# Kernel optimization log

Measured on AMD Instinct MI355X. Metric: run time of the kernel, lower is better.

The kernel has to match this reference:

```python
import jax, jax.numpy as jnp
import numpy as np

N_HEADS = 16
HEAD_DIM = 64
ROPE_BASE = 10000.0


def _rope_cos_sin(T, d, dtype):
    # GPT-NeoX style: inv_freq over even indices, cos/sin duplicated to full head_dim
    inv_freq = 1.0 / (ROPE_BASE ** (jnp.arange(0, d, 2, dtype=jnp.float32) / d))
    freqs = jnp.arange(T, dtype=jnp.float32)[:, None] * inv_freq[None, :]  # [T, d/2]
    emb = jnp.concatenate([freqs, freqs], axis=-1)  # [T, d]
    return jnp.cos(emb).astype(dtype), jnp.sin(emb).astype(dtype)


def _rotate_half(x):
    x1, x2 = jnp.split(x, 2, axis=-1)
    return jnp.concatenate([-x2, x1], axis=-1)


def setup_inputs() -> dict:
    key = jax.random.key(0)
    k1, k2, k3 = jax.random.split(key, 3)
    B, T, C = 2, 2048, 1024
    x = jax.random.normal(k1, (B, T, C), dtype=jnp.float32)
    Wqkv = jax.random.normal(k2, (C, 3 * C), dtype=jnp.float32) * (1.0 / np.sqrt(C))
    Wout = jax.random.normal(k3, (C, C), dtype=jnp.float32) * (1.0 / np.sqrt(C))
    return {"x": x, "Wqkv": Wqkv, "Wout": Wout}


def reference(x, Wqkv, Wout):
    B, T, C = x.shape
    H, D = N_HEADS, HEAD_DIM
    qkv = (x @ Wqkv).reshape(B, T, 3, H, D)
    q, k, v = qkv[:, :, 0], qkv[:, :, 1], qkv[:, :, 2]  # [B,T,H,D]
    q = q.transpose(0, 2, 1, 3)  # [B,H,T,D]
    k = k.transpose(0, 2, 1, 3)
    v = v.transpose(0, 2, 1, 3)
    cos, sin = _rope_cos_sin(T, D, x.dtype)  # [T,D]
    cos = cos[None, None]
    sin = sin[None, None]
    q = q * cos + _rotate_half(q) * sin
    k = k * cos + _rotate_half(k) * sin
    scale = 1.0 / np.sqrt(D)
    scores = jnp.einsum("bhqd,bhkd->bhqk", q, k) * scale  # [B,H,T,T]
    causal = jnp.tril(jnp.ones((T, T), dtype=bool))
    scores = jnp.where(causal[None, None], scores, jnp.finfo(scores.dtype).min)
    attn = jax.nn.softmax(scores, axis=-1)
    out = jnp.einsum("bhqk,bhkd->bhqd", attn, v)  # [B,H,T,D]
    out = out.transpose(0, 2, 1, 3).reshape(B, T, C)
    return out @ Wout
```

## Files before the change

kernel.cpp:

```cpp
#include <hip/hip_runtime.h>


#define B_  2
#define T_  2048
#define C_  1024
#define H_  16
#define D_  64
#define N3_ 3072

typedef unsigned short ushortx8 __attribute__((ext_vector_type(8)));
typedef unsigned short ushortx4 __attribute__((ext_vector_type(4)));
typedef short bf16x8 __attribute__((ext_vector_type(8)));
typedef float f32x4 __attribute__((ext_vector_type(4)));
typedef float f32x16 __attribute__((ext_vector_type(16)));
typedef unsigned int uintx2 __attribute__((ext_vector_type(2)));

__device__ __forceinline__ unsigned short f2bf(float f) {
  union { float f; unsigned u; } v; v.f = f;
  unsigned r = v.u + 0x7FFFu + ((v.u >> 16) & 1u);
  return (unsigned short)(r >> 16);
}
__device__ __forceinline__ float bf2f(unsigned short h) {
  union { unsigned u; float f; } v; v.u = ((unsigned)h) << 16;
  return v.f;
}
__device__ __forceinline__ unsigned cvtpk_bf16(float lo, float hi) {
  unsigned r; asm("v_cvt_pk_bf16_f32 %0, %1, %2" : "=v"(r) : "v"(lo), "v"(hi));
  return r;
}
__device__ __forceinline__ void gload_lds16(const void* g, void* l) {
  __builtin_amdgcn_global_load_lds((const __attribute__((address_space(1))) void*)g,
                                   (__attribute__((address_space(3))) void*)l,
                                   16, 0, 0);
}

__global__ __launch_bounds__(256) void prep_kernel(const float* __restrict__ x,
                                                   unsigned short* __restrict__ Xb,
                                                   const float* __restrict__ Wqkv,
                                                   unsigned short* __restrict__ WqkvT,
                                                   const float* __restrict__ Wout,
                                                   unsigned short* __restrict__ WoutT) {
  __shared__ float tile[32][33];
  const int bid = blockIdx.x;
  if (bid < 4096) {
    size_t i = ((size_t)bid * 256 + threadIdx.x) * 4;
    const float4 v = *(const float4*)(x + i);
    ushortx4 o;
    o[0] = f2bf(v.x); o[1] = f2bf(v.y); o[2] = f2bf(v.z); o[3] = f2bf(v.w);
    *(ushortx4*)(Xb + i) = o;
    return;
  }
  const float* W;
  unsigned short* WT;
  int K, N, n0, k0;
  if (bid < 7168) {
    const int idx = bid - 4096;
    W = Wqkv; WT = WqkvT; K = C_; N = N3_;
    n0 = (idx % (N3_ / 32)) * 32; k0 = (idx / (N3_ / 32)) * 32;
  } else {
    const int idx = bid - 7168;
    W = Wout; WT = WoutT; K = C_; N = C_;
    n0 = (idx % (C_ / 32)) * 32; k0 = (idx / (C_ / 32)) * 32;
  }
  const int tx = threadIdx.x & 31, ty = threadIdx.x >> 5;
#pragma unroll
  for (int i = 0; i < 4; ++i)
    tile[ty + i * 8][tx] = W[(size_t)(k0 + ty + i * 8) * N + n0 + tx];
  __syncthreads();
#pragma unroll
  for (int i = 0; i < 4; ++i)
    WT[(size_t)(n0 + ty + i * 8) * K + k0 + tx] = f2bf(tile[tx][ty + i * 8]);
}

template <int OUTF32>
__global__ __launch_bounds__(256) void gemm_bt_kernel(const unsigned short* __restrict__ A,
                                                      const unsigned short* __restrict__ BT,
                                                      void* __restrict__ Cptr,
                                                      int M, int N, int K) {
  __shared__ unsigned short Alds[128 * 64];
  __shared__ unsigned short Blds[128 * 64];
  const int tid = threadIdx.x;
  const int w = tid >> 6, l = tid & 63;
  const int wr = w >> 1, wc = w & 1;
  const int lg = l >> 4, lr = l & 15;
  const int m0 = blockIdx.y * 128, n0 = blockIdx.x * 128;
  const int lr8 = l >> 3;
  const int lc8 = (l & 7) ^ lr8;

  f32x4 acc[4][4];
#pragma unroll
  for (int i = 0; i < 4; ++i)
#pragma unroll
    for (int j = 0; j < 4; ++j) acc[i][j] = f32x4{0.f, 0.f, 0.f, 0.f};

  for (int k0 = 0; k0 < K; k0 += 64) {
    __syncthreads();
#pragma unroll
    for (int i = 0; i < 4; ++i) {
      const int ch = w * 4 + i;
      gload_lds16(A + (size_t)(m0 + ch * 8 + lr8) * K + k0 + lc8 * 8, &Alds[ch * 512]);
      gload_lds16(BT + (size_t)(n0 + ch * 8 + lr8) * K + k0 + lc8 * 8, &Blds[ch * 512]);
    }
    __syncthreads();
#pragma unroll
    for (int kc = 0; kc < 2; ++kc) {
      bf16x8 af[4], bfr[4];
#pragma unroll
      for (int mi = 0; mi < 4; ++mi) {
        const int row = wr * 64 + mi * 16 + lr;
        const int c16 = (kc * 4 + lg) ^ (row & 7);
        af[mi] = *(const bf16x8*)(&Alds[row * 64 + c16 * 8]);
      }
#pragma unroll
      for (int nj = 0; nj < 4; ++nj) {
        const int row = wc * 64 + nj * 16 + lr;
        const int c16 = (kc * 4 + lg) ^ (row & 7);
        bfr[nj] = *(const bf16x8*)(&Blds[row * 64 + c16 * 8]);
      }
#pragma unroll
      for (int mi = 0; mi < 4; ++mi)
#pragma unroll
        for (int nj = 0; nj < 4; ++nj)
          acc[mi][nj] = __builtin_amdgcn_mfma_f32_16x16x32_bf16(af[mi], bfr[nj], acc[mi][nj], 0, 0, 0);
    }
  }
#pragma unroll
  for (int mi = 0; mi < 4; ++mi)
#pragma unroll
    for (int nj = 0; nj < 4; ++nj)
#pragma unroll
      for (int j = 0; j < 4; ++j) {
        const int row = m0 + wr * 64 + mi * 16 + lg * 4 + j;
        const int col = n0 + wc * 64 + nj * 16 + lr;
        if (OUTF32) ((float*)Cptr)[(size_t)row * N + col] = acc[mi][nj][j];
        else ((unsigned short*)Cptr)[(size_t)row * N + col] = f2bf(acc[mi][nj][j]);
      }
}

__global__ __launch_bounds__(256) void rope_vtrans_kernel(const unsigned short* __restrict__ QKV,
                                                          unsigned short* __restrict__ Qp,
                                                          unsigned short* __restrict__ Kp,
                                                          unsigned short* __restrict__ Vt) {
  __shared__ unsigned short tile[64][72];
  const int tt = blockIdx.x, bh = blockIdx.y;
  const int b = bh >> 4, h = bh & 15;
  const int tid = threadIdx.x;
  if (blockIdx.z == 0) {
    const int half = tid >> 7;
    const int r = (tid >> 1) & 63;
    const int d0 = (tid & 1) * 16;
    const int t = tt * 64 + r;
    const unsigned short* src = QKV + (size_t)(b * T_ + t) * N3_ + half * C_ + h * D_;
    ushortx8 lo0 = *(const ushortx8*)(src + d0);
    ushortx8 lo1 = *(const ushortx8*)(src + d0 + 8);
    ushortx8 hi0 = *(const ushortx8*)(src + d0 + 32);
    ushortx8 hi1 = *(const ushortx8*)(src + d0 + 40);
    ushortx8 olo0, olo1, ohi0, ohi1;
    const float scale = half ? 1.0f : 0.18033688011112042f;
    const float tf = (float)t;
#pragma unroll
    for (int jj = 0; jj < 16; ++jj) {
      const int d = d0 + jj;
      const float invf = exp2f((float)d * -0.41524101186092036f);
      const float ang = tf * invf;
      const float c = cosf(ang), s = sinf(ang);
      const float xl = bf2f(jj < 8 ? lo0[jj] : lo1[jj - 8]);
      const float xh = bf2f(jj < 8 ? hi0[jj] : hi1[jj - 8]);
      const unsigned short rl = f2bf((xl * c - xh * s) * scale);
      const unsigned short rh = f2bf((xh * c + xl * s) * scale);
      if (jj < 8) { olo0[jj] = rl; ohi0[jj] = rh; }
      else        { olo1[jj - 8] = rl; ohi1[jj - 8] = rh; }
    }
    unsigned short* dst = (half ? Kp : Qp) + ((size_t)bh * T_ + t) * D_;
    *(ushortx8*)(dst + d0) = olo0;
    *(ushortx8*)(dst + d0 + 8) = olo1;
    *(ushortx8*)(dst + d0 + 32) = ohi0;
    *(ushortx8*)(dst + d0 + 40) = ohi1;
  } else {
    {
      const int r = tid >> 2, seg = tid & 3;
      const unsigned short* src = QKV + (size_t)(b * T_ + tt * 64 + r) * N3_ + 2 * C_ + h * D_ + seg * 16;
      *(ushortx8*)(&tile[r][seg * 16]) = *(const ushortx8*)(src);
      *(ushortx8*)(&tile[r][seg * 16 + 8]) = *(const ushortx8*)(src + 8);
    }
    __syncthreads();
    {
      const int d = tid >> 2, ts = tid & 3;
      ushortx8 o0, o1;
#pragma unroll
      for (int i = 0; i < 8; ++i) { o0[i] = tile[ts * 16 + i][d]; o1[i] = tile[ts * 16 + 8 + i][d]; }
      unsigned short* dst = Vt + ((size_t)bh * D_ + d) * T_ + tt * 64 + ts * 16;
      *(ushortx8*)(dst) = o0;
      *(ushortx8*)(dst + 8) = o1;
    }
  }
}

__global__ __launch_bounds__(256, 2) void attn10_kernel(const unsigned short* __restrict__ Qp,
                                                        const unsigned short* __restrict__ Kp,
                                                        const unsigned short* __restrict__ Vt,
                                                        unsigned short* __restrict__ Ob) {
  __shared__ unsigned short Klds[2][128 * 64];
  __shared__ unsigned short Vlds[2][64 * 128];
  const int tid = threadIdx.x, w = tid >> 6, l = tid & 63;
  const int lq = l & 31, hi = l >> 5;
  const int swz = lq & 7;
  const int bid = blockIdx.x;
  const int bh = bid & 31;
  const int j = bid >> 5;
  const int g = (j < 8) ? (15 - j) : (j - 8);
  const int q0 = (4 * g + w) * 32;
  const int nt = g + 1;
  const size_t koff = (size_t)bh * T_ * D_;
  const unsigned short* Kb = Kp + koff;
  const unsigned short* Vb = Vt + (size_t)bh * D_ * T_;

  const int lr8 = l >> 3;
  const int lc8 = (l & 7) ^ lr8;
  const int vrl = l >> 4;
  const int vsl = l & 15;

  bf16x8 qf[4];
  {
    const unsigned short* qp = Qp + koff + (size_t)(q0 + lq) * D_ + hi * 8;
#pragma unroll
    for (int ds = 0; ds < 4; ++ds) qf[ds] = *(const bf16x8*)(qp + ds * 16);
  }
  f32x16 o0, o1;
#pragma unroll
  for (int r = 0; r < 16; ++r) { o0[r] = 0.f; o1[r] = 0.f; }
  float m = -3.0e38f, lden = 0.f;

  auto stage = [&](int buf, int kv0s) {
#pragma unroll
    for (int i = 0; i < 4; ++i) {
      const int c = w * 4 + i;
      gload_lds16(Kb + (size_t)(kv0s + c * 8 + lr8) * D_ + lc8 * 8, &Klds[buf][c * 512]);
    }
#pragma unroll
    for (int i = 0; i < 4; ++i) {
      const int c = w * 4 + i;
      const int vr = c * 4 + vrl;
      const int vs = vsl ^ (vr & 7);
      gload_lds16(Vb + (size_t)vr * T_ + kv0s + vs * 8, &Vlds[buf][c * 512]);
    }
  };
  auto pack2 = [&](const f32x16& p, bf16x8& fa, bf16x8& fb) {
    unsigned W0 = cvtpk_bf16(p[0], p[1]), W1 = cvtpk_bf16(p[2], p[3]);
    unsigned W2 = cvtpk_bf16(p[4], p[5]), W3 = cvtpk_bf16(p[6], p[7]);
    uintx2 Aa = __builtin_amdgcn_permlane32_swap(W0, W2, false, false);
    uintx2 Ab = __builtin_amdgcn_permlane32_swap(W1, W3, false, false);
    union { unsigned u[4]; bf16x8 v; } t1 = {{Aa.x, Ab.x, Aa.y, Ab.y}};
    fa = t1.v;
    W0 = cvtpk_bf16(p[8], p[9]);   W1 = cvtpk_bf16(p[10], p[11]);
    W2 = cvtpk_bf16(p[12], p[13]); W3 = cvtpk_bf16(p[14], p[15]);
    Aa = __builtin_amdgcn_permlane32_swap(W0, W2, false, false);
    Ab = __builtin_amdgcn_permlane32_swap(W1, W3, false, false);
    union { unsigned u[4]; bf16x8 v; } t2 = {{Aa.x, Ab.x, Aa.y, Ab.y}};
    fb = t2.v;
  };

  stage(0, 0);

  for (int kt = 0; kt < nt; ++kt) {
    const int cur = kt & 1, nxt = cur ^ 1;
    __builtin_amdgcn_s_barrier();
    const int ktn = (kt + 1 < nt) ? kt + 1 : kt;
    stage(nxt, ktn * 128);
    asm volatile("s_waitcnt vmcnt(8)" ::: "memory");
    __builtin_amdgcn_s_barrier();
    __builtin_amdgcn_sched_barrier(0);

    const unsigned short* KL = &Klds[cur][0];
    const unsigned short* VL = &Vlds[cur][0];
    const int kv0 = kt * 128;
    f32x16 a0, a1, a2, a3;
#pragma unroll
    for (int r = 0; r < 16; ++r) { a0[r] = 0.f; a1[r] = 0.f; a2[r] = 0.f; a3[r] = 0.f; }
    __builtin_amdgcn_s_setprio(1);
#pragma unroll
    for (int ds = 0; ds < 4; ++ds) {
      const int slot = ((ds * 2 + hi) ^ swz) * 8;
      const bf16x8 k0f = *(const bf16x8*)(&KL[(lq) * 64 + slot]);
      const bf16x8 k1f = *(const bf16x8*)(&KL[(32 + lq) * 64 + slot]);
      const bf16x8 k2f = *(const bf16x8*)(&KL[(64 + lq) * 64 + slot]);
      const bf16x8 k3f = *(const bf16x8*)(&KL[(96 + lq) * 64 + slot]);
      a0 = __builtin_amdgcn_mfma_f32_32x32x16_bf16(k0f, qf[ds], a0, 0, 0, 0);
      a1 = __builtin_amdgcn_mfma_f32_32x32x16_bf16(k1f, qf[ds], a1, 0, 0, 0);
      a2 = __builtin_amdgcn_mfma_f32_32x32x16_bf16(k2f, qf[ds], a2, 0, 0, 0);
      a3 = __builtin_amdgcn_mfma_f32_32x32x16_bf16(k3f, qf[ds], a3, 0, 0, 0);
    }
    __builtin_amdgcn_s_setprio(0);
    if (kv0 + 127 > q0) {
      const int thr = q0 + lq - kv0;
#pragma unroll
      for (int r = 0; r < 16; ++r) {
        const int kvloc = (r & 3) + 8 * (r >> 2) + 4 * hi;
        if (kvloc > thr)      a0[r] = -3.0e38f;
        if (kvloc > thr - 32) a1[r] = -3.0e38f;
        if (kvloc > thr - 64) a2[r] = -3.0e38f;
        if (kvloc > thr - 96) a3[r] = -3.0e38f;
      }
    }
    float mx[8];
#pragma unroll
    for (int i = 0; i < 8; ++i)
      mx[i] = fmaxf(fmaxf(fmaxf(a0[i], a0[i + 8]), fmaxf(a1[i], a1[i + 8])),
                    fmaxf(fmaxf(a2[i], a2[i + 8]), fmaxf(a3[i], a3[i + 8])));
#pragma unroll
    for (int i = 0; i < 4; ++i) mx[i] = fmaxf(mx[i], mx[i + 4]);
    const float mloc = fmaxf(fmaxf(mx[0], mx[1]), fmaxf(mx[2], mx[3]));
    const uintx2 mp = __builtin_amdgcn_permlane32_swap(__float_as_uint(mloc), __float_as_uint(mloc), false, false);
    const float pm = fmaxf(__uint_as_float(mp.x), __uint_as_float(mp.y));
    const bool grow = pm > m + 8.0f;
    if (__any(grow)) {
      const float mn = grow ? pm : m;
      const float alpha = __builtin_amdgcn_exp2f(m - mn);
      m = mn;
      lden *= alpha;
#pragma unroll
      for (int r = 0; r < 16; ++r) { o0[r] *= alpha; o1[r] *= alpha; }
    }
#pragma unroll
    for (int r = 0; r < 16; ++r) {
      a0[r] = __builtin_amdgcn_exp2f(a0[r] - m);
      a1[r] = __builtin_amdgcn_exp2f(a1[r] - m);
      a2[r] = __builtin_amdgcn_exp2f(a2[r] - m);
      a3[r] = __builtin_amdgcn_exp2f(a3[r] - m);
    }
    bf16x8 f0, f1, f2, f3, f4, f5, f6, f7;
    pack2(a0, f0, f1); pack2(a1, f2, f3); pack2(a2, f4, f5); pack2(a3, f6, f7);
    __builtin_amdgcn_s_setprio(1);
#pragma unroll
    for (int dt = 0; dt < 2; ++dt) {
      const int rowb = (dt * 32 + lq) * 128;
      const bf16x8 v0 = *(const bf16x8*)(&VL[rowb + ((0 * 2 + hi) ^ swz) * 8]);
      const bf16x8 v1 = *(const bf16x8*)(&VL[rowb + ((1 * 2 + hi) ^ swz) * 8]);
      const bf16x8 v2 = *(const bf16x8*)(&VL[rowb + ((2 * 2 + hi) ^ swz) * 8]);
      const bf16x8 v3 = *(const bf16x8*)(&VL[rowb + ((3 * 2 + hi) ^ swz) * 8]);
      const bf16x8 v4 = *(const bf16x8*)(&VL[rowb + ((4 * 2 + hi) ^ swz) * 8]);
      const bf16x8 v5 = *(const bf16x8*)(&VL[rowb + ((5 * 2 + hi) ^ swz) * 8]);
      const bf16x8 v6 = *(const bf16x8*)(&VL[rowb + ((6 * 2 + hi) ^ swz) * 8]);
      const bf16x8 v7 = *(const bf16x8*)(&VL[rowb + ((7 * 2 + hi) ^ swz) * 8]);
      if (dt == 0) {
        o0 = __builtin_amdgcn_mfma_f32_32x32x16_bf16(v0, f0, o0, 0, 0, 0);
        o0 = __builtin_amdgcn_mfma_f32_32x32x16_bf16(v1, f1, o0, 0, 0, 0);
        o0 = __builtin_amdgcn_mfma_f32_32x32x16_bf16(v2, f2, o0, 0, 0, 0);
        o0 = __builtin_amdgcn_mfma_f32_32x32x16_bf16(v3, f3, o0, 0, 0, 0);
        o0 = __builtin_amdgcn_mfma_f32_32x32x16_bf16(v4, f4, o0, 0, 0, 0);
        o0 = __builtin_amdgcn_mfma_f32_32x32x16_bf16(v5, f5, o0, 0, 0, 0);
        o0 = __builtin_amdgcn_mfma_f32_32x32x16_bf16(v6, f6, o0, 0, 0, 0);
        o0 = __builtin_amdgcn_mfma_f32_32x32x16_bf16(v7, f7, o0, 0, 0, 0);
      } else {
        o1 = __builtin_amdgcn_mfma_f32_32x32x16_bf16(v0, f0, o1, 0, 0, 0);
        o1 = __builtin_amdgcn_mfma_f32_32x32x16_bf16(v1, f1, o1, 0, 0, 0);
        o1 = __builtin_amdgcn_mfma_f32_32x32x16_bf16(v2, f2, o1, 0, 0, 0);
        o1 = __builtin_amdgcn_mfma_f32_32x32x16_bf16(v3, f3, o1, 0, 0, 0);
        o1 = __builtin_amdgcn_mfma_f32_32x32x16_bf16(v4, f4, o1, 0, 0, 0);
        o1 = __builtin_amdgcn_mfma_f32_32x32x16_bf16(v5, f5, o1, 0, 0, 0);
        o1 = __builtin_amdgcn_mfma_f32_32x32x16_bf16(v6, f6, o1, 0, 0, 0);
        o1 = __builtin_amdgcn_mfma_f32_32x32x16_bf16(v7, f7, o1, 0, 0, 0);
      }
    }
    __builtin_amdgcn_s_setprio(0);
    float sm[8];
#pragma unroll
    for (int i = 0; i < 8; ++i)
      sm[i] = ((a0[i] + a0[i + 8]) + (a1[i] + a1[i + 8])) +
              ((a2[i] + a2[i + 8]) + (a3[i] + a3[i + 8]));
#pragma unroll
    for (int i = 0; i < 4; ++i) sm[i] = sm[i] + sm[i + 4];
    const float sloc = (sm[0] + sm[1]) + (sm[2] + sm[3]);
    const uintx2 sp = __builtin_amdgcn_permlane32_swap(__float_as_uint(sloc), __float_as_uint(sloc), false, false);
    lden += __uint_as_float(sp.x) + __uint_as_float(sp.y);
  }
  asm volatile("s_waitcnt vmcnt(0)" ::: "memory");

  const float rl = __builtin_amdgcn_rcpf(lden);
  const int b = bh >> 4, hh = bh & 15;
  unsigned short* orow = Ob + (size_t)(b * T_ + q0 + lq) * C_ + hh * D_ + 4 * hi;
#pragma unroll
  for (int rq = 0; rq < 4; ++rq) {
    ushortx4 ov0, ov1;
#pragma unroll
    for (int i = 0; i < 4; ++i) {
      ov0[i] = f2bf(o0[rq * 4 + i] * rl);
      ov1[i] = f2bf(o1[rq * 4 + i] * rl);
    }
    *(ushortx4*)(orow + rq * 8) = ov0;
    *(ushortx4*)(orow + 32 + rq * 8) = ov1;
  }
}

extern "C" void kernel_launch(void* const* d_in, const int* in_sizes, int n_in,
                              void* d_out, int out_size, void* d_ws, size_t ws_size,
                              hipStream_t stream) {
  const float* x = (const float*)d_in[0];
  const float* Wqkv = (const float*)d_in[1];
  const float* Wout = (const float*)d_in[2];
  float* out = (float*)d_out;
  char* ws = (char*)d_ws;
  unsigned short* Xb    = (unsigned short*)(ws);
  unsigned short* WqkvT = (unsigned short*)(ws + (8ull << 20));
  unsigned short* WoutT = (unsigned short*)(ws + (14ull << 20));
  unsigned short* QKVb  = (unsigned short*)(ws + (16ull << 20));
  unsigned short* Qp    = (unsigned short*)(ws + (40ull << 20));
  unsigned short* Kp    = (unsigned short*)(ws + (48ull << 20));
  unsigned short* Vt    = (unsigned short*)(ws + (56ull << 20));
  unsigned short* Ob    = (unsigned short*)(ws + (64ull << 20));

  prep_kernel<<<8192, 256, 0, stream>>>(x, Xb, Wqkv, WqkvT, Wout, WoutT);
  gemm_bt_kernel<0><<<dim3(N3_ / 128, (B_ * T_) / 128), 256, 0, stream>>>(
      Xb, WqkvT, QKVb, B_ * T_, N3_, C_);
  rope_vtrans_kernel<<<dim3(T_ / 64, B_ * H_, 2), 256, 0, stream>>>(QKVb, Qp, Kp, Vt);
  attn10_kernel<<<512, 256, 0, stream>>>(Qp, Kp, Vt, Ob);
  gemm_bt_kernel<1><<<dim3(C_ / 128, (B_ * T_) / 128), 256, 0, stream>>>(
      Ob, WoutT, out, B_ * T_, C_, C_);
}
```

Before: 114.9 us.

## Fuse RoPE and V transpose into QKV GEMM epilogue

The QKV projection GEMM now applies rotary embedding and Q scaling directly in its epilogue, writing Qp and Kp in head-major layout and V transposed, and the separate rope/transpose kernel is removed. This drops one kernel launch and a full round trip of the QKV intermediate through global memory. In exchange the epilogue issues scattered 2-byte stores for Q/K and computes sin/cos per element inside the GEMM, which may make the epilogue heavier and less coalesced.

```diff
diff --git a/kernel.cpp b/kernel.cpp
--- a/kernel.cpp
+++ b/kernel.cpp
@@ -72,10 +72,104 @@
     WT[(size_t)(n0 + ty + i * 8) * K + k0 + tx] = f2bf(tile[tx][ty + i * 8]);
 }
 
-template <int OUTF32>
+__global__ __launch_bounds__(256) void gemm_rope_kernel(const unsigned short* __restrict__ A,
+                                                        const unsigned short* __restrict__ BT,
+                                                        unsigned short* __restrict__ Qp,
+                                                        unsigned short* __restrict__ Kp,
+                                                        unsigned short* __restrict__ Vt) {
+  const int M = B_ * T_, N = N3_, K = C_;
+  __shared__ unsigned short Alds[128 * 64];
+  __shared__ unsigned short Blds[128 * 64];
+  const int tid = threadIdx.x;
+  const int w = tid >> 6, l = tid & 63;
+  const int wr = w >> 1, wc = w & 1;
+  const int lg = l >> 4, lr = l & 15;
+  const int m0 = blockIdx.y * 128, n0 = blockIdx.x * 128;
+  const int lr8 = l >> 3;
+  const int lc8 = (l & 7) ^ lr8;
+
+  f32x4 acc[4][4];
+#pragma unroll
+  for (int i = 0; i < 4; ++i)
+#pragma unroll
+    for (int j = 0; j < 4; ++j) acc[i][j] = f32x4{0.f, 0.f, 0.f, 0.f};
+
+  for (int k0 = 0; k0 < K; k0 += 64) {
+    __syncthreads();
+#pragma unroll
+    for (int i = 0; i < 4; ++i) {
+      const int ch = w * 4 + i;
+      gload_lds16(A + (size_t)(m0 + ch * 8 + lr8) * K + k0 + lc8 * 8, &Alds[ch * 512]);
+      gload_lds16(BT + (size_t)(n0 + ch * 8 + lr8) * K + k0 + lc8 * 8, &Blds[ch * 512]);
+    }
+    __syncthreads();
+#pragma unroll
+    for (int kc = 0; kc < 2; ++kc) {
+      bf16x8 af[4], bfr[4];
+#pragma unroll
+      for (int mi = 0; mi < 4; ++mi) {
+        const int row = wr * 64 + mi * 16 + lr;
+        const int c16 = (kc * 4 + lg) ^ (row & 7);
+        af[mi] = *(const bf16x8*)(&Alds[row * 64 + c16 * 8]);
+      }
+#pragma unroll
+      for (int nj = 0; nj < 4; ++nj) {
+        const int row = wc * 64 + nj * 16 + lr;
+        const int c16 = (kc * 4 + lg) ^ (row & 7);
+        bfr[nj] = *(const bf16x8*)(&Blds[row * 64 + c16 * 8]);
+      }
+#pragma unroll
+      for (int mi = 0; mi < 4; ++mi)
+#pragma unroll
+        for (int nj = 0; nj < 4; ++nj)
+          acc[mi][nj] = __builtin_amdgcn_mfma_f32_16x16x32_bf16(af[mi], bfr[nj], acc[mi][nj], 0, 0, 0);
+    }
+  }
+  const int half = n0 >> 10;
+  const int h = ((n0 & 1023) >> 6) + wc;
+  const int b = m0 >> 11;
+  const int t_base = (m0 & 2047) + wr * 64;
+  const int bh = b * H_ + h;
+  if (half < 2) {
+    unsigned short* dst = (half ? Kp : Qp) + (size_t)bh * T_ * D_;
+    const float scale = half ? 1.0f : 0.18033688011112042f;
+#pragma unroll
+    for (int nj = 0; nj < 2; ++nj) {
+      const int d = nj * 16 + lr;
+      const float invf = exp2f((float)d * -0.41524101186092036f);
+#pragma unroll
+      for (int mi = 0; mi < 4; ++mi) {
+#pragma unroll
+        for (int j = 0; j < 4; ++j) {
+          const int t = t_base + mi * 16 + lg * 4 + j;
+          const float ang = (float)t * invf;
+          const float c = cosf(ang), s = sinf(ang);
+          const float lo = acc[mi][nj][j], hi = acc[mi][nj + 2][j];
+          dst[(size_t)t * D_ + d]      = f2bf((lo * c - hi * s) * scale);
+          dst[(size_t)t * D_ + d + 32] = f2bf((hi * c + lo * s) * scale);
+        }
+      }
+    }
+  } else {
+    unsigned short* dst = Vt + (size_t)bh * D_ * T_;
+#pragma unroll
+    for (int mi = 0; mi < 4; ++mi) {
+      const int t0 = t_base + mi * 16 + lg * 4;
+#pragma unroll
+      for (int nj = 0; nj < 4; ++nj) {
+        const int d = nj * 16 + lr;
+        ushortx4 ov;
+#pragma unroll
+        for (int j = 0; j < 4; ++j) ov[j] = f2bf(acc[mi][nj][j]);
+        *(ushortx4*)(dst + (size_t)d * T_ + t0) = ov;
+      }
+    }
+  }
+}
+
 __global__ __launch_bounds__(256) void gemm_bt_kernel(const unsigned short* __restrict__ A,
                                                       const unsigned short* __restrict__ BT,
-                                                      void* __restrict__ Cptr,
+                                                      float* __restrict__ Cptr,
                                                       int M, int N, int K) {
   __shared__ unsigned short Alds[128 * 64];
   __shared__ unsigned short Blds[128 * 64];
@@ -132,68 +226,8 @@
       for (int j = 0; j < 4; ++j) {
         const int row = m0 + wr * 64 + mi * 16 + lg * 4 + j;
         const int col = n0 + wc * 64 + nj * 16 + lr;
-        if (OUTF32) ((float*)Cptr)[(size_t)row * N + col] = acc[mi][nj][j];
-        else ((unsigned short*)Cptr)[(size_t)row * N + col] = f2bf(acc[mi][nj][j]);
-      }
-}
-
-__global__ __launch_bounds__(256) void rope_vtrans_kernel(const unsigned short* __restrict__ QKV,
-                                                          unsigned short* __restrict__ Qp,
-                                                          unsigned short* __restrict__ Kp,
-                                                          unsigned short* __restrict__ Vt) {
-  __shared__ unsigned short tile[64][72];
-  const int tt = blockIdx.x, bh = blockIdx.y;
-  const int b = bh >> 4, h = bh & 15;
-  const int tid = threadIdx.x;
-  if (blockIdx.z == 0) {
-    const int half = tid >> 7;
-    const int r = (tid >> 1) & 63;
-    const int d0 = (tid & 1) * 16;
-    const int t = tt * 64 + r;
-    const unsigned short* src = QKV + (size_t)(b * T_ + t) * N3_ + half * C_ + h * D_;
-    ushortx8 lo0 = *(const ushortx8*)(src + d0);
-    ushortx8 lo1 = *(const ushortx8*)(src + d0 + 8);
-    ushortx8 hi0 = *(const ushortx8*)(src + d0 + 32);
-    ushortx8 hi1 = *(const ushortx8*)(src + d0 + 40);
-    ushortx8 olo0, olo1, ohi0, ohi1;
-    const float scale = half ? 1.0f : 0.18033688011112042f;
-    const float tf = (float)t;
-#pragma unroll
-    for (int jj = 0; jj < 16; ++jj) {
-      const int d = d0 + jj;
-      const float invf = exp2f((float)d * -0.41524101186092036f);
-      const float ang = tf * invf;
-      const float c = cosf(ang), s = sinf(ang);
-      const float xl = bf2f(jj < 8 ? lo0[jj] : lo1[jj - 8]);
-      const float xh = bf2f(jj < 8 ? hi0[jj] : hi1[jj - 8]);
-      const unsigned short rl = f2bf((xl * c - xh * s) * scale);
-      const unsigned short rh = f2bf((xh * c + xl * s) * scale);
-      if (jj < 8) { olo0[jj] = rl; ohi0[jj] = rh; }
-      else        { olo1[jj - 8] = rl; ohi1[jj - 8] = rh; }
-    }
-    unsigned short* dst = (half ? Kp : Qp) + ((size_t)bh * T_ + t) * D_;
-    *(ushortx8*)(dst + d0) = olo0;
-    *(ushortx8*)(dst + d0 + 8) = olo1;
-    *(ushortx8*)(dst + d0 + 32) = ohi0;
-    *(ushortx8*)(dst + d0 + 40) = ohi1;
-  } else {
-    {
-      const int r = tid >> 2, seg = tid & 3;
-      const unsigned short* src = QKV + (size_t)(b * T_ + tt * 64 + r) * N3_ + 2 * C_ + h * D_ + seg * 16;
-      *(ushortx8*)(&tile[r][seg * 16]) = *(const ushortx8*)(src);
-      *(ushortx8*)(&tile[r][seg * 16 + 8]) = *(const ushortx8*)(src + 8);
-    }
-    __syncthreads();
-    {
-      const int d = tid >> 2, ts = tid & 3;
-      ushortx8 o0, o1;
-#pragma unroll
-      for (int i = 0; i < 8; ++i) { o0[i] = tile[ts * 16 + i][d]; o1[i] = tile[ts * 16 + 8 + i][d]; }
-      unsigned short* dst = Vt + ((size_t)bh * D_ + d) * T_ + tt * 64 + ts * 16;
-      *(ushortx8*)(dst) = o0;
-      *(ushortx8*)(dst + 8) = o1;
-    }
-  }
+        Cptr[(size_t)row * N + col] = acc[mi][nj][j];
+      }
 }
 
 __global__ __launch_bounds__(256, 2) void attn10_kernel(const unsigned short* __restrict__ Qp,
@@ -403,17 +437,15 @@
   unsigned short* Xb    = (unsigned short*)(ws);
   unsigned short* WqkvT = (unsigned short*)(ws + (8ull << 20));
   unsigned short* WoutT = (unsigned short*)(ws + (14ull << 20));
-  unsigned short* QKVb  = (unsigned short*)(ws + (16ull << 20));
   unsigned short* Qp    = (unsigned short*)(ws + (40ull << 20));
   unsigned short* Kp    = (unsigned short*)(ws + (48ull << 20));
   unsigned short* Vt    = (unsigned short*)(ws + (56ull << 20));
   unsigned short* Ob    = (unsigned short*)(ws + (64ull << 20));
 
   prep_kernel<<<8192, 256, 0, stream>>>(x, Xb, Wqkv, WqkvT, Wout, WoutT);
-  gemm_bt_kernel<0><<<dim3(N3_ / 128, (B_ * T_) / 128), 256, 0, stream>>>(
-      Xb, WqkvT, QKVb, B_ * T_, N3_, C_);
-  rope_vtrans_kernel<<<dim3(T_ / 64, B_ * H_, 2), 256, 0, stream>>>(QKVb, Qp, Kp, Vt);
+  gemm_rope_kernel<<<dim3(N3_ / 128, (B_ * T_) / 128), 256, 0, stream>>>(
+      Xb, WqkvT, Qp, Kp, Vt);
   attn10_kernel<<<512, 256, 0, stream>>>(Qp, Kp, Vt, Ob);
-  gemm_bt_kernel<1><<<dim3(C_ / 128, (B_ * T_) / 128), 256, 0, stream>>>(
+  gemm_bt_kernel<<<dim3(C_ / 128, (B_ * T_) / 128), 256, 0, stream>>>(
       Ob, WoutT, out, B_ * T_, C_, C_);
 }
```

After: 367.8 us. +220.0%, slower.
